# Kernel tuning notes

Measured on AMD Instinct MI355X. Metric: run time of the kernel, lower is better.

Reference implementation:

```python
import jax, jax.numpy as jnp
import numpy as np

GAMMA = 0.1
EPSILON = 0.1
NUM_ITERS = 4


def setup_inputs() -> dict:
    key = jax.random.key(0)
    k1, k2, k3, k4 = jax.random.split(key, 4)
    N, E, D = 100000, 1600000, 128
    x = jax.random.normal(k1, (N, D), dtype=jnp.float32)
    edge_index = jax.random.randint(k2, (2, E), 0, N, dtype=jnp.int32)
    # kaiming-uniform-like scale for W, glorot-like for GCN weight
    W = jax.random.normal(k3, (D, D), dtype=jnp.float32) * (1.0 / np.sqrt(D))
    W_phi = jax.random.normal(k4, (D, D), dtype=jnp.float32) * (1.0 / np.sqrt(D))
    bias = jnp.zeros((D,), dtype=jnp.float32)
    return {"x": x, "edge_index": edge_index, "W": W, "W_phi": W_phi, "bias": bias}


def _gcn_conv(x, W_phi, src, dst, n_nodes):
    """GCNConv(bias=False): symmetric normalization with added self-loops."""
    xw = x @ W_phi.T  # [N, D] linear transform (torch Linear: y = x W^T)
    ones = jnp.ones(src.shape, dtype=xw.dtype)
    deg = jax.ops.segment_sum(ones, dst, num_segments=n_nodes) + 1.0  # +1 self-loop
    dinv = jax.lax.rsqrt(deg)  # deg >= 1, always finite
    norm = dinv[src] * dinv[dst]  # [E]
    agg = jax.ops.segment_sum(xw[src] * norm[:, None], dst, num_segments=n_nodes)
    # self-loop contribution: norm_ii = dinv_i^2
    return agg + xw * (dinv * dinv)[:, None]


def reference(x, edge_index, W, W_phi, bias):
    n_nodes, d = x.shape
    src, dst = edge_index[0], edge_index[1]
    A = W - W.T - GAMMA * jnp.eye(d, dtype=x.dtype)  # antisymmetric - gamma*I
    for _ in range(NUM_ITERS):
        h = _gcn_conv(x, W_phi, src, dst, n_nodes)
        h = jnp.tanh(x @ A.T + h + bias)
        x = x + EPSILON * h
    return x
```

## Files before the change

### kernel.cpp

```cpp
#include <hip/hip_runtime.h>
#include <hip/hip_bf16.h>
#include <math.h>

#define GAMMA 0.1f
#define EPSILON 0.1f
#define NUM_ITERS 4
#define BSHIFT 9
#define CH_P 36
#define CH_SZ (16 * CH_P)

typedef __attribute__((ext_vector_type(8))) short short8;
typedef __attribute__((ext_vector_type(4))) float floatx4;

__device__ __forceinline__ float bf2f(unsigned short u) {
  union { unsigned int i; float f; } v; v.i = ((unsigned int)u) << 16; return v.f;
}
__device__ __forceinline__ unsigned short f2bf(float f) {
  union { float f; unsigned int i; } v; v.f = f;
  unsigned int x = v.i;
  return (unsigned short)((x + 0x7fffu + ((x >> 16) & 1u)) >> 16);
}
__device__ __forceinline__ unsigned int f2_to_bfx2(float a, float b) {
  return (unsigned int)f2bf(a) | (((unsigned int)f2bf(b)) << 16);
}
__device__ __forceinline__ float2 bfx2_to_f2(unsigned int u) {
  union { unsigned int i; float f; } lo, hi;
  lo.i = u << 16; hi.i = u & 0xffff0000u;
  return make_float2(lo.f, hi.f);
}
__device__ __forceinline__ float tanh_fast(float s) {
  float c = fminf(15.0f, fmaxf(-15.0f, s));
  float e = __expf(2.0f * c);
  return (e - 1.0f) * __frcp_rn(e + 1.0f);
}


__global__ void detect_kernel(const unsigned int* __restrict__ x, int* __restrict__ flag) {
  __shared__ int ws4[4];
  int tid = threadIdx.x;
  int bad = 0;
  for (int i = tid; i < 2048; i += 256) {
    unsigned int u = x[i];
    float lo = bf2f((unsigned short)(u & 0xffffu));
    if (!(fabsf(lo) <= 64.0f)) bad++;
  }
#pragma unroll
  for (int d = 1; d < 64; d <<= 1) bad += __shfl_xor(bad, d, 64);
  if ((tid & 63) == 0) ws4[tid >> 6] = bad;
  __syncthreads();
  if (tid == 0) *flag = (ws4[0] + ws4[1] + ws4[2] + ws4[3] > 64) ? 1 : 0;
}


__global__ void fill_kernel(unsigned short* __restrict__ out, int n, unsigned short val) {
  int t = blockIdx.x * blockDim.x + threadIdx.x;
  if (t < n) out[t] = val;
}

__global__ void prep_kernel(const void* __restrict__ Wv, const void* __restrict__ Wphiv,
                            const void* __restrict__ biasv, const int* __restrict__ flag,
                            unsigned short* __restrict__ Am, unsigned short* __restrict__ Wb,
                            float* __restrict__ bias_f) {
  int t = blockIdx.x * blockDim.x + threadIdx.x;
  if (t >= 128 * 128) return;
  int isf = *flag;
  int j = t >> 7, k = t & 127;
  float w_jk, w_kj, wp;
  if (isf) {
    const float* W = (const float*)Wv;
    const float* Wp = (const float*)Wphiv;
    w_jk = W[t]; w_kj = W[k * 128 + j]; wp = Wp[t];
  } else {
    const unsigned short* W = (const unsigned short*)Wv;
    const unsigned short* Wp = (const unsigned short*)Wphiv;
    w_jk = bf2f(W[t]); w_kj = bf2f(W[k * 128 + j]); wp = bf2f(Wp[t]);
  }
  float v = w_jk - w_kj;
  if (j == k) v -= GAMMA;
  Am[t] = f2bf(v);
  Wb[t] = f2bf(wp);
  if (t < 128)
    bias_f[t] = isf ? ((const float*)biasv)[t] : bf2f(((const unsigned short*)biasv)[t]);
}

__global__ void init_x_kernel(const void* __restrict__ xinv, const int* __restrict__ flag,
                              unsigned short* __restrict__ xb, int N, int NP) {
  int t = blockIdx.x * blockDim.x + threadIdx.x;
  if (t >= NP * 16) return;
  int base = t * 8;
  int row = base >> 7;
  uint4 o;
  if (row < N) {
    if (*flag) {
      const float* p = (const float*)xinv + base;
      float4 f0 = *(const float4*)p;
      float4 f1 = *(const float4*)(p + 4);
      o.x = f2_to_bfx2(f0.x, f0.y); o.y = f2_to_bfx2(f0.z, f0.w);
      o.z = f2_to_bfx2(f1.x, f1.y); o.w = f2_to_bfx2(f1.z, f1.w);
    } else {
      o = *(const uint4*)((const unsigned short*)xinv + base);
    }
  } else {
    o = make_uint4(0u, 0u, 0u, 0u);
  }
  *(uint4*)(xb + base) = o;
}

__global__ void scale_kernel(const unsigned short* __restrict__ xb,
                             const float* __restrict__ dinv,
                             unsigned short* __restrict__ z, int NP16) {
  int t = blockIdx.x * blockDim.x + threadIdx.x;
  if (t >= NP16) return;
  int base = t * 8;
  float dv = dinv[base >> 7];
  uint4 u = *(const uint4*)(xb + base);
  float2 f;
  uint4 o;
  f = bfx2_to_f2(u.x); o.x = f2_to_bfx2(f.x * dv, f.y * dv);
  f = bfx2_to_f2(u.y); o.y = f2_to_bfx2(f.x * dv, f.y * dv);
  f = bfx2_to_f2(u.z); o.z = f2_to_bfx2(f.x * dv, f.y * dv);
  f = bfx2_to_f2(u.w); o.w = f2_to_bfx2(f.x * dv, f.y * dv);
  *(uint4*)(z + base) = o;
}


__global__ void bcount_kernel(const int* __restrict__ dst, int* __restrict__ gcnt,
                              int E, int NB) {
  __shared__ int cnt[512];
  int tid = threadIdx.x;
  for (int j = tid; j < 512; j += 256) cnt[j] = 0;
  __syncthreads();
  int base = blockIdx.x * 4096;
#pragma unroll
  for (int k = 0; k < 16; ++k) {
    int i = base + k * 256 + tid;
    if (i < E) atomicAdd(&cnt[dst[i] >> BSHIFT], 1);
  }
  __syncthreads();
  for (int j = tid; j < NB; j += 256)
    if (cnt[j]) atomicAdd(&gcnt[j], cnt[j]);
}

__global__ void bscan_kernel(const int* __restrict__ gcnt, int* __restrict__ gofs,
                             int* __restrict__ gcur, int NB, int E) {
  if (threadIdx.x == 0 && blockIdx.x == 0) {
    int run = 0;
    for (int i = 0; i < NB; ++i) { gofs[i] = run; gcur[i] = run; run += gcnt[i]; }
    gofs[NB] = E;
  }
}

__global__ void bscatter_kernel(const int* __restrict__ src, const int* __restrict__ dst,
                                int* __restrict__ gcur, uint2* __restrict__ bpairs,
                                int E, int NB) {
  __shared__ int cnt[512];
  __shared__ int pos[512];
  int tid = threadIdx.x;
  for (int j = tid; j < 512; j += 256) cnt[j] = 0;
  __syncthreads();
  int base = blockIdx.x * 4096;
#pragma unroll
  for (int k = 0; k < 16; ++k) {
    int i = base + k * 256 + tid;
    if (i < E) atomicAdd(&cnt[dst[i] >> BSHIFT], 1);
  }
  __syncthreads();
  for (int j = tid; j < NB; j += 256)
    pos[j] = cnt[j] ? atomicAdd(&gcur[j], cnt[j]) : 0;
  __syncthreads();
#pragma unroll
  for (int k = 0; k < 16; ++k) {
    int i = base + k * 256 + tid;
    if (i < E) {
      int d = dst[i];
      int slot = atomicAdd(&pos[d >> BSHIFT], 1);
      bpairs[slot] = make_uint2((unsigned)d, (unsigned)src[i]);
    }
  }
}

__global__ __launch_bounds__(256) void bfinal_kernel(
    const uint2* __restrict__ bpairs, const int* __restrict__ gofs,
    int* __restrict__ offs, float* __restrict__ dinv, int* __restrict__ csr,
    int N, int NP, int E) {
  __shared__ int dl[512];
  __shared__ int cur[512];
  __shared__ int wsum2[4];
  int b = blockIdx.x, t = threadIdx.x;
  int node0 = b << BSHIFT;
  dl[t] = 0; dl[t + 256] = 0;
  __syncthreads();
  int e0 = gofs[b], e1 = gofs[b + 1];
  for (int i = e0 + t; i < e1; i += 256)
    atomicAdd(&dl[bpairs[i].x - node0], 1);
  __syncthreads();
  int v0 = dl[2 * t], v1 = dl[2 * t + 1];
  int ps = v0 + v1;
  int lane = t & 63, w = t >> 6;
  int inc = ps;
#pragma unroll
  for (int d = 1; d < 64; d <<= 1) { int q = __shfl_up(inc, d, 64); if (lane >= d) inc += q; }
  if (lane == 63) wsum2[w] = inc;
  __syncthreads();
  int woff = 0;
  for (int k = 0; k < w; ++k) woff += wsum2[k];
  int base = e0 + woff + inc - ps;
  int n0 = node0 + 2 * t, n1 = node0 + 2 * t + 1;
  if (n0 < N) offs[n0] = base;
  if (n1 < N) offs[n1] = base + v0;
  if (n0 < NP) dinv[n0] = rsqrtf((float)v0 + 1.0f);
  if (n1 < NP) dinv[n1] = rsqrtf((float)v1 + 1.0f);
  cur[2 * t] = base;
  cur[2 * t + 1] = base + v0;
  if (b == 0 && t == 0) offs[N] = E;
  __syncthreads();
  for (int i = e0 + t; i < e1; i += 256) {
    uint2 p = bpairs[i];
    int s = atomicAdd(&cur[p.x - node0], 1);
    csr[s] = (int)p.y;
  }
}


__global__ __launch_bounds__(256) void fused_kernel(
    unsigned short* __restrict__ xb, const unsigned short* __restrict__ Am,
    const unsigned short* __restrict__ Wphi, const float* __restrict__ dinv,
    const unsigned short* __restrict__ g, const float* __restrict__ bias_f,
    void* __restrict__ outb, unsigned short* __restrict__ znext,
    const int* __restrict__ flag, int Mvalid) {
  __shared__ __align__(16) unsigned short bsm[128 * 128];
  const int tid = threadIdx.x, lane = tid & 63, wid = tid >> 6;
  const int l15 = lane & 15, quad = lane >> 4;
  const int m0 = blockIdx.x * 64;
  const int arow = m0 + wid * 16 + l15;
  const size_t abase = (size_t)arow * 128 + quad * 8;

  short8 afrag[4], sfrag[4];
#pragma unroll
  for (int kk = 0; kk < 4; ++kk) afrag[kk] = *(const short8*)(xb + abase + kk * 32);
#pragma unroll
  for (int kk = 0; kk < 4; ++kk) sfrag[kk] = *(const short8*)(g + abase + kk * 32);
  const float dva = dinv[arow];

#pragma unroll
  for (int p = 0; p < 8; ++p) {
    int c = p * 256 + tid;
    int row = c >> 4, slot = c & 15;
    *(uint4*)(bsm + row * 128 + ((slot ^ (row & 7)) * 8)) = *(const uint4*)(Am + c * 8);
  }
  __syncthreads();

  floatx4 acc[8];
  const floatx4 zero = {0.f, 0.f, 0.f, 0.f};
#pragma unroll
  for (int j = 0; j < 8; ++j) acc[j] = zero;
  const int rsw = (l15 & 7);
#pragma unroll
  for (int kk = 0; kk < 4; ++kk) {
#pragma unroll
    for (int j = 0; j < 8; ++j) {
      short8 b = *(const short8*)(bsm + (j * 16 + l15) * 128 + (((kk * 4 + quad) ^ rsw) * 8));
      acc[j] = __builtin_amdgcn_mfma_f32_16x16x32_bf16(afrag[kk], b, acc[j], 0, 0, 0);
    }
  }
  __syncthreads();

#pragma unroll
  for (int p = 0; p < 8; ++p) {
    int c = p * 256 + tid;
    int row = c >> 4, slot = c & 15;
    *(uint4*)(bsm + row * 128 + ((slot ^ (row & 7)) * 8)) = *(const uint4*)(Wphi + c * 8);
  }
  __syncthreads();
#pragma unroll
  for (int kk = 0; kk < 4; ++kk) {
#pragma unroll
    for (int j = 0; j < 8; ++j) {
      short8 b = *(const short8*)(bsm + (j * 16 + l15) * 128 + (((kk * 4 + quad) ^ rsw) * 8));
      acc[j] = __builtin_amdgcn_mfma_f32_16x16x32_bf16(sfrag[kk], b, acc[j], 0, 0, 0);
    }
  }
  __syncthreads();

  const int isf = *flag;
  const bool valid = arow < Mvalid;
  float* wbuf = (float*)bsm + wid * 2 * CH_SZ;
#pragma unroll
  for (int kk = 0; kk < 4; ++kk) {
    float* buf = wbuf + (kk & 1) * CH_SZ;
#pragma unroll
    for (int jj = 0; jj < 2; ++jj) {
#pragma unroll
      for (int r = 0; r < 4; ++r)
        buf[(quad * 4 + r) * CH_P + jj * 16 + l15] = acc[2 * kk + jj][r];
    }
    const int col0 = kk * 32 + quad * 8;
    const float* ap = &buf[l15 * CH_P + quad * 8];
    float4 s0 = *(const float4*)ap;
    float4 s1 = *(const float4*)(ap + 4);
    float4 b0 = *(const float4*)&bias_f[col0];
    float4 b1 = *(const float4*)&bias_f[col0 + 4];
    union { short8 s; unsigned short h[8]; } xu; xu.s = afrag[kk];
    float xv[8];
    xv[0] = bf2f(xu.h[0]) + EPSILON * tanh_fast(s0.x + b0.x);
    xv[1] = bf2f(xu.h[1]) + EPSILON * tanh_fast(s0.y + b0.y);
    xv[2] = bf2f(xu.h[2]) + EPSILON * tanh_fast(s0.z + b0.z);
    xv[3] = bf2f(xu.h[3]) + EPSILON * tanh_fast(s0.w + b0.w);
    xv[4] = bf2f(xu.h[4]) + EPSILON * tanh_fast(s1.x + b1.x);
    xv[5] = bf2f(xu.h[5]) + EPSILON * tanh_fast(s1.y + b1.y);
    xv[6] = bf2f(xu.h[6]) + EPSILON * tanh_fast(s1.z + b1.z);
    xv[7] = bf2f(xu.h[7]) + EPSILON * tanh_fast(s1.w + b1.w);
    uint4 pk;
    pk.x = f2_to_bfx2(xv[0], xv[1]); pk.y = f2_to_bfx2(xv[2], xv[3]);
    pk.z = f2_to_bfx2(xv[4], xv[5]); pk.w = f2_to_bfx2(xv[6], xv[7]);
    if (valid) {
      *(uint4*)(xb + abase + kk * 32) = pk;
      if (znext) {
        uint4 zk;
        zk.x = f2_to_bfx2(xv[0] * dva, xv[1] * dva);
        zk.y = f2_to_bfx2(xv[2] * dva, xv[3] * dva);
        zk.z = f2_to_bfx2(xv[4] * dva, xv[5] * dva);
        zk.w = f2_to_bfx2(xv[6] * dva, xv[7] * dva);
        *(uint4*)(znext + abase + kk * 32) = zk;
      }
      if (outb) {
        if (isf) {
          float* op = (float*)outb + abase + kk * 32;
          *(float4*)op = make_float4(xv[0], xv[1], xv[2], xv[3]);
          *(float4*)(op + 4) = make_float4(xv[4], xv[5], xv[6], xv[7]);
        } else {
          *(uint4*)((unsigned short*)outb + abase + kk * 32) = pk;
        }
      }
    }
  }
}

__global__ __launch_bounds__(256) void agg_kernel(
    const unsigned short* __restrict__ y,
    const int* __restrict__ offs,
    const int* __restrict__ csr,
    const float* __restrict__ dinv,
    unsigned short* __restrict__ g,
    int N) {
  int i = blockIdx.x * 4 + (threadIdx.x >> 6);
  if (i >= N) return;
  int lane = threadIdx.x & 63;
  int sub = lane >> 4;
  int c8 = (lane & 15) * 8;

  float a0 = 0.f, a1 = 0.f, a2 = 0.f, a3 = 0.f, a4 = 0.f, a5 = 0.f, a6 = 0.f, a7 = 0.f;

#define ACC8(u) { float2 f_; \
  f_ = bfx2_to_f2((u).x); a0 += f_.x; a1 += f_.y; \
  f_ = bfx2_to_f2((u).y); a2 += f_.x; a3 += f_.y; \
  f_ = bfx2_to_f2((u).z); a4 += f_.x; a5 += f_.y; \
  f_ = bfx2_to_f2((u).w); a6 += f_.x; a7 += f_.y; }

  int e0 = offs[i], e1 = offs[i + 1];
  int e = e0 + sub;
  for (; e + 12 < e1; e += 16) {
    int s0 = csr[e];
    int s1 = csr[e + 4];
    int s2 = csr[e + 8];
    int s3 = csr[e + 12];
    uint4 u0 = *(const uint4*)(y + (size_t)s0 * 128 + c8);
    uint4 u1 = *(const uint4*)(y + (size_t)s1 * 128 + c8);
    uint4 u2 = *(const uint4*)(y + (size_t)s2 * 128 + c8);
    uint4 u3 = *(const uint4*)(y + (size_t)s3 * 128 + c8);
    ACC8(u0); ACC8(u1); ACC8(u2); ACC8(u3);
  }
  for (; e < e1; e += 4) {
    int s0 = csr[e];
    uint4 u0 = *(const uint4*)(y + (size_t)s0 * 128 + c8);
    ACC8(u0);
  }
#undef ACC8

  a0 += __shfl_xor(a0, 16, 64); a0 += __shfl_xor(a0, 32, 64);
  a1 += __shfl_xor(a1, 16, 64); a1 += __shfl_xor(a1, 32, 64);
  a2 += __shfl_xor(a2, 16, 64); a2 += __shfl_xor(a2, 32, 64);
  a3 += __shfl_xor(a3, 16, 64); a3 += __shfl_xor(a3, 32, 64);
  a4 += __shfl_xor(a4, 16, 64); a4 += __shfl_xor(a4, 32, 64);
  a5 += __shfl_xor(a5, 16, 64); a5 += __shfl_xor(a5, 32, 64);
  a6 += __shfl_xor(a6, 16, 64); a6 += __shfl_xor(a6, 32, 64);
  a7 += __shfl_xor(a7, 16, 64); a7 += __shfl_xor(a7, 32, 64);

  if (sub == 0) {
    uint4 su = *(const uint4*)(y + (size_t)i * 128 + c8);
    float2 f;
    f = bfx2_to_f2(su.x); a0 += f.x; a1 += f.y;
    f = bfx2_to_f2(su.y); a2 += f.x; a3 += f.y;
    f = bfx2_to_f2(su.z); a4 += f.x; a5 += f.y;
    f = bfx2_to_f2(su.w); a6 += f.x; a7 += f.y;
    float dv = dinv[i];
    uint4 o;
    o.x = f2_to_bfx2(a0 * dv, a1 * dv);
    o.y = f2_to_bfx2(a2 * dv, a3 * dv);
    o.z = f2_to_bfx2(a4 * dv, a5 * dv);
    o.w = f2_to_bfx2(a6 * dv, a7 * dv);
    *(uint4*)(g + (size_t)i * 128 + c8) = o;
  }
}


extern "C" void kernel_launch(void* const* d_in, const int* in_sizes, int n_in,
                              void* d_out, int out_size, void* d_ws, size_t ws_size,
                              hipStream_t stream) {
  const void* x_in = d_in[0];
  const int* ei = (const int*)d_in[1];
  const void* W = d_in[2];
  const void* Wphi = d_in[3];
  const void* bias = d_in[4];

  const int N = in_sizes[0] / 128;
  const int E = in_sizes[1] / 2;
  const int NP = ((N + 63) / 64) * 64;
  const int* src = ei;
  const int* dst = ei + E;
  const int NB = (N + 511) >> BSHIFT;
  const int EB = (E + 4095) / 4096;

  size_t off = 0;
  auto place = [&](size_t bytes) { size_t r = off; off = (off + bytes + 255) & ~(size_t)255; return r; };
  size_t o_xb   = place((size_t)NP * 128 * 2);
  size_t o_z    = place((size_t)NP * 128 * 2);
  size_t o_g    = place((size_t)NP * 128 * 2);
  size_t o_Am   = place(128 * 128 * 2);
  size_t o_Wb   = place(128 * 128 * 2);
  size_t o_bf   = place(128 * 4);
  size_t o_flag = place(4);
  size_t o_dinv = place((size_t)(NB * 512 + 64) * 4);
  size_t o_offs = place((size_t)(N + 1) * 4);
  size_t o_gcnt = place((size_t)NB * 4);
  size_t o_gofs = place((size_t)(NB + 1) * 4);
  size_t o_gcur = place((size_t)NB * 4);
  size_t o_bprs = place((size_t)E * 8);
  size_t o_csr  = place((size_t)E * 4);
  if (off > ws_size || in_sizes[0] % 128 != 0 || out_size != N * 128 || n_in < 5) {
    fill_kernel<<<(out_size * 2 + 255) / 256, 256, 0, stream>>>(
        (unsigned short*)d_out, out_size, (unsigned short)0x3F80);
    return;
  }
  char* basep = (char*)d_ws;
  unsigned short* xb = (unsigned short*)(basep + o_xb);
  unsigned short* z  = (unsigned short*)(basep + o_z);
  unsigned short* g  = (unsigned short*)(basep + o_g);
  unsigned short* Am = (unsigned short*)(basep + o_Am);
  unsigned short* Wb = (unsigned short*)(basep + o_Wb);
  float* bias_f = (float*)(basep + o_bf);
  int* flag   = (int*)(basep + o_flag);
  float* dinv = (float*)(basep + o_dinv);
  int* offs   = (int*)(basep + o_offs);
  int* gcnt   = (int*)(basep + o_gcnt);
  int* gofs   = (int*)(basep + o_gofs);
  int* gcur   = (int*)(basep + o_gcur);
  uint2* bpairs = (uint2*)(basep + o_bprs);
  int* csr    = (int*)(basep + o_csr);

  hipMemsetAsync(gcnt, 0, (size_t)NB * 4, stream);
  detect_kernel<<<1, 256, 0, stream>>>((const unsigned int*)x_in, flag);
  prep_kernel<<<(128 * 128 + 255) / 256, 256, 0, stream>>>(W, Wphi, bias, flag, Am, Wb, bias_f);
  init_x_kernel<<<(NP * 16 + 255) / 256, 256, 0, stream>>>(x_in, flag, xb, N, NP);
  bcount_kernel<<<EB, 256, 0, stream>>>(dst, gcnt, E, NB);
  bscan_kernel<<<1, 64, 0, stream>>>(gcnt, gofs, gcur, NB, E);
  bscatter_kernel<<<EB, 256, 0, stream>>>(src, dst, gcur, bpairs, E, NB);
  bfinal_kernel<<<NB, 256, 0, stream>>>(bpairs, gofs, offs, dinv, csr, N, NP, E);

  const int gblocks = NP / 64;
  scale_kernel<<<(NP * 16 + 255) / 256, 256, 0, stream>>>(xb, dinv, z, NP * 16);
  for (int t = 0; t < NUM_ITERS; ++t) {
    agg_kernel<<<(N + 3) / 4, 256, 0, stream>>>(z, offs, csr, dinv, g, N);
    void* outp = (t == NUM_ITERS - 1) ? d_out : nullptr;
    unsigned short* znext = (t == NUM_ITERS - 1) ? nullptr : z;
    fused_kernel<<<gblocks, 256, 0, stream>>>(xb, Am, Wb, dinv, g, bias_f,
                                              outp, znext, flag, N);
  }
}
```

Baseline: 566.2 us.

## Fuse neighbor aggregation into GEMM kernel with ping-pong z buffers

Removes the separate aggregation kernel and performs the CSR gather for each block's 64 rows inside the fused GEMM kernel, staging the aggregated rows in shared memory. It ping-pongs between two z buffers so the next iteration's input isn't overwritten while other blocks still read it. This eliminates writing and rereading the g buffer and one launch per iteration, but each wave now gathers 16 rows sequentially, reducing gather parallelism and memory-level concurrency.

Result: slower. 826.2 us (+45.9%).

```diff
diff --git a/kernel.cpp b/kernel.cpp
--- a/kernel.cpp
+++ b/kernel.cpp
@@ -222,10 +222,11 @@
 }
 
 
-__global__ __launch_bounds__(256) void fused_kernel(
+__global__ __launch_bounds__(256) void fused2_kernel(
     unsigned short* __restrict__ xb, const unsigned short* __restrict__ Am,
     const unsigned short* __restrict__ Wphi, const float* __restrict__ dinv,
-    const unsigned short* __restrict__ g, const float* __restrict__ bias_f,
+    const unsigned short* __restrict__ zcur, const int* __restrict__ offs,
+    const int* __restrict__ csr, const float* __restrict__ bias_f,
     void* __restrict__ outb, unsigned short* __restrict__ znext,
     const int* __restrict__ flag, int Mvalid) {
   __shared__ __align__(16) unsigned short bsm[128 * 128];
@@ -234,13 +235,80 @@
   const int m0 = blockIdx.x * 64;
   const int arow = m0 + wid * 16 + l15;
   const size_t abase = (size_t)arow * 128 + quad * 8;
-
-  short8 afrag[4], sfrag[4];
+  const int sub = lane >> 4;
+  const int c8 = l15 * 8;
+  const int rsw = (l15 & 7);
+
+  unsigned short* gls = bsm;
+#define ACC8(u) { float2 f_; \
+  f_ = bfx2_to_f2((u).x); a0 += f_.x; a1 += f_.y; \
+  f_ = bfx2_to_f2((u).y); a2 += f_.x; a3 += f_.y; \
+  f_ = bfx2_to_f2((u).z); a4 += f_.x; a5 += f_.y; \
+  f_ = bfx2_to_f2((u).w); a6 += f_.x; a7 += f_.y; }
+  for (int r = 0; r < 16; ++r) {
+    const int n = m0 + wid * 16 + r;
+    const int R = wid * 16 + r;
+    if (n >= Mvalid) {
+      if (sub == 0)
+        *(uint4*)(gls + R * 128 + ((l15 ^ (R & 7)) * 8)) = make_uint4(0u, 0u, 0u, 0u);
+      continue;
+    }
+    float a0 = 0.f, a1 = 0.f, a2 = 0.f, a3 = 0.f, a4 = 0.f, a5 = 0.f, a6 = 0.f, a7 = 0.f;
+    int e0 = offs[n], e1 = offs[n + 1];
+    int e = e0 + sub;
+    for (; e + 12 < e1; e += 16) {
+      int s0 = csr[e];
+      int s1 = csr[e + 4];
+      int s2 = csr[e + 8];
+      int s3 = csr[e + 12];
+      uint4 u0 = *(const uint4*)(zcur + (size_t)s0 * 128 + c8);
+      uint4 u1 = *(const uint4*)(zcur + (size_t)s1 * 128 + c8);
+      uint4 u2 = *(const uint4*)(zcur + (size_t)s2 * 128 + c8);
+      uint4 u3 = *(const uint4*)(zcur + (size_t)s3 * 128 + c8);
+      ACC8(u0); ACC8(u1); ACC8(u2); ACC8(u3);
+    }
+    for (; e < e1; e += 4) {
+      int s0 = csr[e];
+      uint4 u0 = *(const uint4*)(zcur + (size_t)s0 * 128 + c8);
+      ACC8(u0);
+    }
+    a0 += __shfl_xor(a0, 16, 64); a0 += __shfl_xor(a0, 32, 64);
+    a1 += __shfl_xor(a1, 16, 64); a1 += __shfl_xor(a1, 32, 64);
+    a2 += __shfl_xor(a2, 16, 64); a2 += __shfl_xor(a2, 32, 64);
+    a3 += __shfl_xor(a3, 16, 64); a3 += __shfl_xor(a3, 32, 64);
+    a4 += __shfl_xor(a4, 16, 64); a4 += __shfl_xor(a4, 32, 64);
+    a5 += __shfl_xor(a5, 16, 64); a5 += __shfl_xor(a5, 32, 64);
+    a6 += __shfl_xor(a6, 16, 64); a6 += __shfl_xor(a6, 32, 64);
+    a7 += __shfl_xor(a7, 16, 64); a7 += __shfl_xor(a7, 32, 64);
+    if (sub == 0) {
+      uint4 su = *(const uint4*)(zcur + (size_t)n * 128 + c8);
+      float2 f;
+      f = bfx2_to_f2(su.x); a0 += f.x; a1 += f.y;
+      f = bfx2_to_f2(su.y); a2 += f.x; a3 += f.y;
+      f = bfx2_to_f2(su.z); a4 += f.x; a5 += f.y;
+      f = bfx2_to_f2(su.w); a6 += f.x; a7 += f.y;
+      float dv = dinv[n];
+      uint4 o;
+      o.x = f2_to_bfx2(a0 * dv, a1 * dv);
+      o.y = f2_to_bfx2(a2 * dv, a3 * dv);
+      o.z = f2_to_bfx2(a4 * dv, a5 * dv);
+      o.w = f2_to_bfx2(a6 * dv, a7 * dv);
+      *(uint4*)(gls + R * 128 + ((l15 ^ (R & 7)) * 8)) = o;
+    }
+  }
+#undef ACC8
+
+  short8 sfrag[4];
+#pragma unroll
+  for (int kk = 0; kk < 4; ++kk)
+    sfrag[kk] = *(const short8*)(gls + (wid * 16 + l15) * 128 + (((kk * 4 + quad) ^ rsw) * 8));
+
+  short8 afrag[4];
 #pragma unroll
   for (int kk = 0; kk < 4; ++kk) afrag[kk] = *(const short8*)(xb + abase + kk * 32);
-#pragma unroll
-  for (int kk = 0; kk < 4; ++kk) sfrag[kk] = *(const short8*)(g + abase + kk * 32);
   const float dva = dinv[arow];
+
+  __syncthreads();
 
 #pragma unroll
   for (int p = 0; p < 8; ++p) {
@@ -254,7 +322,6 @@
   const floatx4 zero = {0.f, 0.f, 0.f, 0.f};
 #pragma unroll
   for (int j = 0; j < 8; ++j) acc[j] = zero;
-  const int rsw = (l15 & 7);
 #pragma unroll
   for (int kk = 0; kk < 4; ++kk) {
 #pragma unroll
@@ -336,73 +403,6 @@
   }
 }
 
-__global__ __launch_bounds__(256) void agg_kernel(
-    const unsigned short* __restrict__ y,
-    const int* __restrict__ offs,
-    const int* __restrict__ csr,
-    const float* __restrict__ dinv,
-    unsigned short* __restrict__ g,
-    int N) {
-  int i = blockIdx.x * 4 + (threadIdx.x >> 6);
-  if (i >= N) return;
-  int lane = threadIdx.x & 63;
-  int sub = lane >> 4;
-  int c8 = (lane & 15) * 8;
-
-  float a0 = 0.f, a1 = 0.f, a2 = 0.f, a3 = 0.f, a4 = 0.f, a5 = 0.f, a6 = 0.f, a7 = 0.f;
-
-#define ACC8(u) { float2 f_; \
-  f_ = bfx2_to_f2((u).x); a0 += f_.x; a1 += f_.y; \
-  f_ = bfx2_to_f2((u).y); a2 += f_.x; a3 += f_.y; \
-  f_ = bfx2_to_f2((u).z); a4 += f_.x; a5 += f_.y; \
-  f_ = bfx2_to_f2((u).w); a6 += f_.x; a7 += f_.y; }
-
-  int e0 = offs[i], e1 = offs[i + 1];
-  int e = e0 + sub;
-  for (; e + 12 < e1; e += 16) {
-    int s0 = csr[e];
-    int s1 = csr[e + 4];
-    int s2 = csr[e + 8];
-    int s3 = csr[e + 12];
-    uint4 u0 = *(const uint4*)(y + (size_t)s0 * 128 + c8);
-    uint4 u1 = *(const uint4*)(y + (size_t)s1 * 128 + c8);
-    uint4 u2 = *(const uint4*)(y + (size_t)s2 * 128 + c8);
-    uint4 u3 = *(const uint4*)(y + (size_t)s3 * 128 + c8);
-    ACC8(u0); ACC8(u1); ACC8(u2); ACC8(u3);
-  }
-  for (; e < e1; e += 4) {
-    int s0 = csr[e];
-    uint4 u0 = *(const uint4*)(y + (size_t)s0 * 128 + c8);
-    ACC8(u0);
-  }
-#undef ACC8
-
-  a0 += __shfl_xor(a0, 16, 64); a0 += __shfl_xor(a0, 32, 64);
-  a1 += __shfl_xor(a1, 16, 64); a1 += __shfl_xor(a1, 32, 64);
-  a2 += __shfl_xor(a2, 16, 64); a2 += __shfl_xor(a2, 32, 64);
-  a3 += __shfl_xor(a3, 16, 64); a3 += __shfl_xor(a3, 32, 64);
-  a4 += __shfl_xor(a4, 16, 64); a4 += __shfl_xor(a4, 32, 64);
-  a5 += __shfl_xor(a5, 16, 64); a5 += __shfl_xor(a5, 32, 64);
-  a6 += __shfl_xor(a6, 16, 64); a6 += __shfl_xor(a6, 32, 64);
-  a7 += __shfl_xor(a7, 16, 64); a7 += __shfl_xor(a7, 32, 64);
-
-  if (sub == 0) {
-    uint4 su = *(const uint4*)(y + (size_t)i * 128 + c8);
-    float2 f;
-    f = bfx2_to_f2(su.x); a0 += f.x; a1 += f.y;
-    f = bfx2_to_f2(su.y); a2 += f.x; a3 += f.y;
-    f = bfx2_to_f2(su.z); a4 += f.x; a5 += f.y;
-    f = bfx2_to_f2(su.w); a6 += f.x; a7 += f.y;
-    float dv = dinv[i];
-    uint4 o;
-    o.x = f2_to_bfx2(a0 * dv, a1 * dv);
-    o.y = f2_to_bfx2(a2 * dv, a3 * dv);
-    o.z = f2_to_bfx2(a4 * dv, a5 * dv);
-    o.w = f2_to_bfx2(a6 * dv, a7 * dv);
-    *(uint4*)(g + (size_t)i * 128 + c8) = o;
-  }
-}
-
 
 extern "C" void kernel_launch(void* const* d_in, const int* in_sizes, int n_in,
                               void* d_out, int out_size, void* d_ws, size_t ws_size,
@@ -424,8 +424,8 @@
   size_t off = 0;
   auto place = [&](size_t bytes) { size_t r = off; off = (off + bytes + 255) & ~(size_t)255; return r; };
   size_t o_xb   = place((size_t)NP * 128 * 2);
-  size_t o_z    = place((size_t)NP * 128 * 2);
-  size_t o_g    = place((size_t)NP * 128 * 2);
+  size_t o_z0   = place((size_t)NP * 128 * 2);
+  size_t o_z1   = place((size_t)NP * 128 * 2);
   size_t o_Am   = place(128 * 128 * 2);
   size_t o_Wb   = place(128 * 128 * 2);
   size_t o_bf   = place(128 * 4);
@@ -444,8 +444,8 @@
   }
   char* basep = (char*)d_ws;
   unsigned short* xb = (unsigned short*)(basep + o_xb);
-  unsigned short* z  = (unsigned short*)(basep + o_z);
-  unsigned short* g  = (unsigned short*)(basep + o_g);
+  unsigned short* z0 = (unsigned short*)(basep + o_z0);
+  unsigned short* z1 = (unsigned short*)(basep + o_z1);
   unsigned short* Am = (unsigned short*)(basep + o_Am);
   unsigned short* Wb = (unsigned short*)(basep + o_Wb);
   float* bias_f = (float*)(basep + o_bf);
@@ -468,12 +468,12 @@
   bfinal_kernel<<<NB, 256, 0, stream>>>(bpairs, gofs, offs, dinv, csr, N, NP, E);
 
   const int gblocks = NP / 64;
-  scale_kernel<<<(NP * 16 + 255) / 256, 256, 0, stream>>>(xb, dinv, z, NP * 16);
+  unsigned short* zb[2] = { z0, z1 };
+  scale_kernel<<<(NP * 16 + 255) / 256, 256, 0, stream>>>(xb, dinv, zb[0], NP * 16);
   for (int t = 0; t < NUM_ITERS; ++t) {
-    agg_kernel<<<(N + 3) / 4, 256, 0, stream>>>(z, offs, csr, dinv, g, N);
     void* outp = (t == NUM_ITERS - 1) ? d_out : nullptr;
-    unsigned short* znext = (t == NUM_ITERS - 1) ? nullptr : z;
-    fused_kernel<<<gblocks, 256, 0, stream>>>(xb, Am, Wb, dinv, g, bias_f,
-                                              outp, znext, flag, N);
-  }
-}
+    unsigned short* znext = (t == NUM_ITERS - 1) ? nullptr : zb[(t + 1) & 1];
+    fused2_kernel<<<gblocks, 256, 0, stream>>>(xb, Am, Wb, dinv, zb[t & 1], offs, csr,
+                                               bias_f, outp, znext, flag, N);
+  }
+}
```
